# Optimization experiments

Measured on AMD Instinct MI355X. Metric: run time of the kernel, lower is better.

Reference implementation:

```python
import jax, jax.numpy as jnp
import numpy as np

EPS = 1e-5

def _ln(x, g, b):
    m = jnp.mean(x, axis=-1, keepdims=True)
    v = jnp.mean((x - m) ** 2, axis=-1, keepdims=True)
    return (x - m) * jax.lax.rsqrt(v + EPS) * g + b


def setup_inputs() -> dict:
    key = jax.random.key(0)
    B, T, C, H, A = 4, 1024, 1024, 16, 64
    ks = jax.random.split(key, 16)
    s = 0.02
    inp = {
        "x": jax.random.normal(ks[0], (B, T, C), jnp.float32),
        "ln1_g": jnp.ones((C,), jnp.float32), "ln1_b": jnp.zeros((C,), jnp.float32),
        "ln2_g": jnp.ones((C,), jnp.float32), "ln2_b": jnp.zeros((C,), jnp.float32),
        "ln3_g": jnp.ones((C,), jnp.float32), "ln3_b": jnp.zeros((C,), jnp.float32),
        "wq": jax.random.normal(ks[1], (C, C), jnp.float32) * s, "bq": jnp.zeros((C,), jnp.float32),
        "wk": jax.random.normal(ks[2], (C, C), jnp.float32) * s, "bk": jnp.zeros((C,), jnp.float32),
        "wv": jax.random.normal(ks[3], (C, C), jnp.float32) * s, "bv": jnp.zeros((C,), jnp.float32),
        "wo": jax.random.normal(ks[4], (C, C), jnp.float32) * s, "bo": jnp.zeros((C,), jnp.float32),
        "w1": jax.random.normal(ks[5], (C, 4 * C), jnp.float32) * s, "b1": jnp.zeros((4 * C,), jnp.float32),
        "w2": jax.random.normal(ks[6], (4 * C, C), jnp.float32) * s, "b2": jnp.zeros((C,), jnp.float32),
        "wd": jax.random.normal(ks[7], (C, A), jnp.float32) * 1e-4, "bd": jnp.zeros((A,), jnp.float32),
        "wu": jax.random.normal(ks[8], (A, C), jnp.float32) * 1e-4, "bu": jnp.zeros((C,), jnp.float32),
    }
    return inp


def _block(x, ln1_g, ln1_b, ln2_g, ln2_b, ln3_g, ln3_b,
           wq, bq, wk, bk, wv, bv, wo, bo, w1, b1, w2, b2, wd, bd, wu, bu):
    B, T, C = x.shape
    H = 16
    D = C // H
    normed = _ln(x, ln3_g, ln3_b)  # ln3 of original input, used by adapter

    # --- causal self-attention on ln1(x) ---
    h = _ln(x, ln1_g, ln1_b)
    q = (h @ wq + bq).reshape(B, T, H, D)
    k = (h @ wk + bk).reshape(B, T, H, D)
    v = (h @ wv + bv).reshape(B, T, H, D)
    att = jnp.einsum('bqhd,bkhd->bhqk', q, k) * (1.0 / np.sqrt(D))
    causal = jnp.tril(jnp.ones((T, T), bool))
    att = jnp.where(causal, att, -jnp.inf)
    att = jax.nn.softmax(att, axis=-1)
    y = jnp.einsum('bhqk,bkhd->bqhd', att, v).reshape(B, T, C)
    attn_out = y @ wo + bo

    hidden = x + attn_out
    # --- MLP on ln2(hidden) ---
    m = _ln(hidden, ln2_g, ln2_b)
    mlp_out = jax.nn.gelu(m @ w1 + b1, approximate=False) @ w2 + b2
    forward_states = hidden + mlp_out

    # --- adapter on ln3(original x) ---
    a = jax.nn.relu(normed @ wd + bd) @ wu + bu

    # dropout is identity (p=0 / eval)
    return hidden + forward_states + a


def reference(x, ln1_g, ln1_b, ln2_g, ln2_b, ln3_g, ln3_b,
              wq, bq, wk, bk, wv, bv, wo, bo, w1, b1, w2, b2, wd, bd, wu, bu):
    return _block(x, ln1_g, ln1_b, ln2_g, ln2_b, ln3_g, ln3_b,
                  wq, bq, wk, bk, wv, bv, wo, bo, w1, b1, w2, b2, wd, bd, wu, bu)
```

## Files before the change

kernel.cpp:

```cpp
#include <hip/hip_runtime.h>

typedef unsigned short u16;
typedef __bf16 bf16x8 __attribute__((ext_vector_type(8)));
typedef u16    u16x8  __attribute__((ext_vector_type(8)));
typedef float  f32x4  __attribute__((ext_vector_type(4)));

__device__ __forceinline__ u16 f2bf(float f) {
    union { float f; unsigned u; } x{f};
    unsigned r = x.u + 0x7fffu + ((x.u >> 16) & 1u);
    return (u16)(r >> 16);
}
__device__ __forceinline__ float bf2f(u16 h) {
    union { unsigned u; float f; } x{(unsigned)h << 16};
    return x.f;
}

__device__ __forceinline__ f32x4 mfma16(bf16x8 a, bf16x8 b, f32x4 c) {
    return __builtin_amdgcn_mfma_f32_16x16x32_bf16(a, b, c, 0, 0, 0);
}

__device__ __forceinline__ void async_ld16(const void* g, void* l) {
    __builtin_amdgcn_global_load_lds(
        (const __attribute__((address_space(1))) unsigned int*)g,
        (__attribute__((address_space(3))) unsigned int*)l, 16, 0, 0);
}

struct PrepParams {
    const float* src[8];
    u16* dst[8];
    int K[8], N[8];
    int pfx[9];
    const float *bq, *bk, *bv;
    float* bqkv;
};

__global__ void prep_kernel(PrepParams p) {
    const int b = blockIdx.x;
    if (b >= p.pfx[8]) {
        int i = (b - p.pfx[8]) * 256 + threadIdx.x;
        p.bqkv[i] = i < 1024 ? p.bq[i] : (i < 2048 ? p.bk[i - 1024] : p.bv[i - 2048]);
        return;
    }
    int j = 0;
    while (b >= p.pfx[j + 1]) ++j;
    const float* __restrict__ in = p.src[j];
    u16* __restrict__ out = p.dst[j];
    const int K = p.K[j], N = p.N[j];
    const int local = b - p.pfx[j];
    const int tx = N >> 6;
    const int n0 = (local % tx) * 64, k0 = (local / tx) * 64;

    __shared__ float tile[64][65];
    const int tid = threadIdx.x;
    const int rr = tid >> 4, cc = tid & 15;
#pragma unroll
    for (int it = 0; it < 4; ++it) {
        const int r = rr + it * 16;
        float4 v = *(const float4*)(in + (long)(k0 + r) * N + n0 + cc * 4);
        tile[r][cc * 4 + 0] = v.x; tile[r][cc * 4 + 1] = v.y;
        tile[r][cc * 4 + 2] = v.z; tile[r][cc * 4 + 3] = v.w;
    }
    __syncthreads();
#pragma unroll
    for (int it = 0; it < 4; ++it) {
        const int n = rr + it * 16;
        ushort4 o;
        o.x = f2bf(tile[cc * 4 + 0][n]);
        o.y = f2bf(tile[cc * 4 + 1][n]);
        o.z = f2bf(tile[cc * 4 + 2][n]);
        o.w = f2bf(tile[cc * 4 + 3][n]);
        *(ushort4*)(out + (long)(n0 + n) * K + k0 + cc * 4) = o;
    }
}

__global__ void ln_dual_kernel(const float* __restrict__ x,
                               const float* __restrict__ g1, const float* __restrict__ b1,
                               const float* __restrict__ g3, const float* __restrict__ b3,
                               u16* __restrict__ out1, u16* __restrict__ out3) {
    const int row = blockIdx.x;
    const long base = (long)row * 1024;
    const int t = threadIdx.x;
    float4 v = ((const float4*)(x + base))[t];
    float s = v.x + v.y + v.z + v.w;
    float ss = v.x * v.x + v.y * v.y + v.z * v.z + v.w * v.w;
    for (int o = 32; o > 0; o >>= 1) { s += __shfl_down(s, o); ss += __shfl_down(ss, o); }
    __shared__ float red[8];
    if ((t & 63) == 0) { red[t >> 6] = s; red[(t >> 6) + 4] = ss; }
    __syncthreads();
    float sum = red[0] + red[1] + red[2] + red[3];
    float sq  = red[4] + red[5] + red[6] + red[7];
    const float mean = sum * (1.f / 1024.f);
    const float rstd = rsqrtf(sq * (1.f / 1024.f) - mean * mean + 1e-5f);
    float4 G1 = ((const float4*)g1)[t], B1 = ((const float4*)b1)[t];
    float4 G3 = ((const float4*)g3)[t], B3 = ((const float4*)b3)[t];
    float n0 = (v.x - mean) * rstd, n1 = (v.y - mean) * rstd;
    float n2 = (v.z - mean) * rstd, n3 = (v.w - mean) * rstd;
    ushort4 o1, o3;
    o1.x = f2bf(n0 * G1.x + B1.x); o1.y = f2bf(n1 * G1.y + B1.y);
    o1.z = f2bf(n2 * G1.z + B1.z); o1.w = f2bf(n3 * G1.w + B1.w);
    o3.x = f2bf(n0 * G3.x + B3.x); o3.y = f2bf(n1 * G3.y + B3.y);
    o3.z = f2bf(n2 * G3.z + B3.z); o3.w = f2bf(n3 * G3.w + B3.w);
    ((ushort4*)(out1 + base))[t] = o1;
    ((ushort4*)(out3 + base))[t] = o3;
}

__global__ void ln_single_kernel(const float* __restrict__ x,
                                 const float* __restrict__ g, const float* __restrict__ b,
                                 u16* __restrict__ out) {
    const int row = blockIdx.x;
    const long base = (long)row * 1024;
    const int t = threadIdx.x;
    float4 v = ((const float4*)(x + base))[t];
    float s = v.x + v.y + v.z + v.w;
    float ss = v.x * v.x + v.y * v.y + v.z * v.z + v.w * v.w;
    for (int o = 32; o > 0; o >>= 1) { s += __shfl_down(s, o); ss += __shfl_down(ss, o); }
    __shared__ float red[8];
    if ((t & 63) == 0) { red[t >> 6] = s; red[(t >> 6) + 4] = ss; }
    __syncthreads();
    float sum = red[0] + red[1] + red[2] + red[3];
    float sq  = red[4] + red[5] + red[6] + red[7];
    const float mean = sum * (1.f / 1024.f);
    const float rstd = rsqrtf(sq * (1.f / 1024.f) - mean * mean + 1e-5f);
    float4 G = ((const float4*)g)[t], B = ((const float4*)b)[t];
    ushort4 o;
    o.x = f2bf((v.x - mean) * rstd * G.x + B.x);
    o.y = f2bf((v.y - mean) * rstd * G.y + B.y);
    o.z = f2bf((v.z - mean) * rstd * G.z + B.z);
    o.w = f2bf((v.w - mean) * rstd * G.w + B.w);
    ((ushort4*)(out + base))[t] = o;
}

__global__ void transpose_v(const u16* __restrict__ qkv, u16* __restrict__ vT) {
    const int bh = blockIdx.z, b = bh >> 4, hh = bh & 15;
    const int t0 = blockIdx.x * 32, d0 = blockIdx.y * 32;
    __shared__ u16 tile[32][33];
    const u16* src = qkv + (long)(b * 1024) * 3072 + 2048 + hh * 64;
    for (int i = threadIdx.y; i < 32; i += 8)
        tile[i][threadIdx.x] = src[(long)(t0 + i) * 3072 + d0 + threadIdx.x];
    __syncthreads();
    u16* dst = vT + (long)bh * 64 * 1024;
    for (int i = threadIdx.y; i < 32; i += 8)
        dst[(long)(d0 + i) * 1024 + t0 + threadIdx.x] = tile[threadIdx.x][i];
}

__global__ void reduce_out4(float* __restrict__ out, const u16* __restrict__ p,
                            const float* __restrict__ b2) {
    const long base = (long)blockIdx.x * 1024;
    const int t = threadIdx.x;
    float4 sum = {0.f, 0.f, 0.f, 0.f};
#pragma unroll
    for (int z = 0; z < 4; ++z) {
        ushort4 q = ((const ushort4*)(p + (long)z * (4096L * 1024) + base))[t];
        sum.x += bf2f(q.x); sum.y += bf2f(q.y);
        sum.z += bf2f(q.z); sum.w += bf2f(q.w);
    }
    float4 bias = ((const float4*)b2)[t];
    float4 o = ((const float4*)(out + base))[t];
    o.x += sum.x + bias.x; o.y += sum.y + bias.y;
    o.z += sum.z + bias.z; o.w += sum.w + bias.w;
    ((float4*)(out + base))[t] = o;
}

template <typename Epi>
__global__ __launch_bounds__(128, 2)
void gemm_big(const u16* __restrict__ A, const u16* __restrict__ Bt,
              int N, int K, int ld, Epi epi) {
    constexpr int AE = 128 * 32;
    __shared__ u16 sm[2][AE + AE];
    const int tid = threadIdx.x;
    const int wid = tid >> 6, lane = tid & 63;
    const int lr = lane & 15, lh = lane >> 4;
    const int m0 = blockIdx.y * 128, n0 = blockIdx.x * 128;
    const long k0g = (long)blockIdx.z * K;
    const int wn = wid * 64;

    const int cr = lane >> 2, lq = lane & 3;
    long aoff[4], boff[4];
    int lA[4], lB[4];
#pragma unroll
    for (int c = 0; c < 4; ++c) {
        const int r = wid * 64 + c * 16 + cr;
        const int q = lq ^ (r & 3) ^ ((r >> 2) & 3);
        aoff[c] = (long)(m0 + r) * ld + k0g + q * 8;
        boff[c] = (long)(n0 + r) * ld + k0g + q * 8;
        lA[c] = (wid * 4 + c) * 512;
        lB[c] = AE + (wid * 4 + c) * 512;
    }
    const int qoff = ((lh ^ (lr & 3) ^ ((lr >> 2) & 3)) & 3) * 8;

    f32x4 acc[8][4] = {};
    const int nk = K / 32;

    auto stage = [&](int kt) {
        const long ko = (long)kt * 32;
        u16* s = sm[kt & 1];
#pragma unroll
        for (int c = 0; c < 4; ++c) {
            async_ld16(A + aoff[c] + ko, s + lA[c]);
            async_ld16(Bt + boff[c] + ko, s + lB[c]);
        }
    };
    auto compute = [&](int kt) {
        const u16* sA = sm[kt & 1];
        const u16* sB = sA + AE;
        bf16x8 bfr[4];
#pragma unroll
        for (int j = 0; j < 4; ++j)
            bfr[j] = *(const bf16x8*)(sB + (wn + j * 16 + lr) * 32 + qoff);
#pragma unroll
        for (int i = 0; i < 8; ++i) {
            bf16x8 af = *(const bf16x8*)(sA + (i * 16 + lr) * 32 + qoff);
#pragma unroll
            for (int j = 0; j < 4; ++j)
                acc[i][j] = mfma16(af, bfr[j], acc[i][j]);
        }
    };

    stage(0);
    __syncthreads();
    for (int kt = 0; kt < nk; ++kt) {
        if (kt + 1 < nk) stage(kt + 1);
        compute(kt);
        __syncthreads();
    }

#pragma unroll
    for (int i = 0; i < 8; ++i)
#pragma unroll
        for (int j = 0; j < 4; ++j) {
            const int col = n0 + wn + j * 16 + lr;
#pragma unroll
            for (int r = 0; r < 4; ++r)
                epi(m0 + i * 16 + lh * 4 + r, col, acc[i][j][r]);
        }
}

template <typename Epi>
__global__ __launch_bounds__(256, 4)
void gemm_64(const u16* __restrict__ A, const u16* __restrict__ Bt,
             int N, int K, int ld, Epi epi) {
    constexpr int AE = 128 * 32;
    constexpr int BE = 64 * 32;
    __shared__ u16 sm[2][AE + BE];
    const int tid = threadIdx.x;
    const int m0 = blockIdx.y * 128;
    const int n0 = blockIdx.x * 64;
    const long k0g = (long)blockIdx.z * K;
    const int wid = tid >> 6, lane = tid & 63;
    const int lr = lane & 15, lh = lane >> 4;
    const int wm = wid * 32;

    const int cr = lane >> 2, lq = lane & 3;
    const int ra0 = wid * 32 + cr, ra1 = ra0 + 16;
    const int qa0 = lq ^ (ra0 & 3) ^ ((ra0 >> 2) & 3);
    const int qa1 = lq ^ (ra1 & 3) ^ ((ra1 >> 2) & 3);
    const long aoff0 = (long)(m0 + ra0) * ld + k0g + qa0 * 8;
    const long aoff1 = (long)(m0 + ra1) * ld + k0g + qa1 * 8;
    const int la0 = wid * 1024, la1 = la0 + 512;

    const int rb = wid * 16 + cr;
    const int qb = lq ^ (rb & 3) ^ ((rb >> 2) & 3);
    const long boff0 = (long)min(n0 + rb, N - 1) * ld + k0g + qb * 8;
    const int lb0 = AE + wid * 512;

    const int qoff = ((lh ^ (lr & 3) ^ ((lr >> 2) & 3)) & 3) * 8;

    f32x4 acc[2][4] = {};
    const int nk = K / 32;

    auto stage = [&](int kt) {
        const long ko = (long)kt * 32;
        u16* s = sm[kt & 1];
        async_ld16(A + aoff0 + ko, s + la0);
        async_ld16(A + aoff1 + ko, s + la1);
        async_ld16(Bt + boff0 + ko, s + lb0);
    };
    auto compute = [&](int kt) {
        const u16* sA = sm[kt & 1];
        const u16* sB = sA + AE;
        bf16x8 af[2], bfr[4];
#pragma unroll
        for (int i = 0; i < 2; ++i)
            af[i] = *(const bf16x8*)(sA + (wm + i * 16 + lr) * 32 + qoff);
#pragma unroll
        for (int j = 0; j < 4; ++j)
            bfr[j] = *(const bf16x8*)(sB + (j * 16 + lr) * 32 + qoff);
#pragma unroll
        for (int i = 0; i < 2; ++i)
#pragma unroll
            for (int j = 0; j < 4; ++j)
                acc[i][j] = mfma16(af[i], bfr[j], acc[i][j]);
    };

    stage(0);
    __syncthreads();
    for (int kt = 0; kt < nk; ++kt) {
        if (kt + 1 < nk) stage(kt + 1);
        compute(kt);
        __syncthreads();
    }

#pragma unroll
    for (int i = 0; i < 2; ++i)
#pragma unroll
        for (int j = 0; j < 4; ++j) {
            const int col = n0 + j * 16 + lr;
            if (col < N) {
#pragma unroll
                for (int r = 0; r < 4; ++r) {
                    const int row = m0 + wm + i * 16 + lh * 4 + r;
                    epi(row, col, acc[i][j][r]);
                }
            }
        }
}

struct EpiBF16Bias {
    u16* out; const float* bias; int ldo;
    __device__ void operator()(int r, int c, float v) const {
        out[(long)r * ldo + c] = f2bf(v + bias[c]);
    }
};
struct EpiResid {
    float* hidden; const float* bias; const float* x;
    __device__ void operator()(int r, int c, float v) const {
        long i = (long)r * 1024 + c; hidden[i] = v + bias[c] + x[i];
    }
};
struct EpiGelu {
    u16* out; const float* bias;
    __device__ void operator()(int r, int c, float v) const {
        float x = v + bias[c];
        float u2 = x * (1.5957691216f + 0.0713548162726f * x * x);
        float g = x / (1.f + __expf(-u2));
        out[(long)r * 4096 + c] = f2bf(g);
    }
};
struct EpiReluBF16 {
    u16* out; const float* bias;
    __device__ void operator()(int r, int c, float v) const {
        out[(long)r * 64 + c] = f2bf(fmaxf(v + bias[c], 0.f));
    }
};
struct EpiAdapter {
    float* out; const float* bias; const float* hidden;
    __device__ void operator()(int r, int c, float v) const {
        long i = (long)r * 1024 + c; out[i] = 2.f * hidden[i] + v + bias[c];
    }
};
struct EpiStoreSplit {
    u16* p;
    __device__ void operator()(int r, int c, float v) const {
        p[(long)blockIdx.z * (4096L * 1024) + (long)r * 1024 + c] = f2bf(v);
    }
};

__global__ __launch_bounds__(256, 2)
void attn_kernel(const u16* __restrict__ qkv, const u16* __restrict__ vT,
                 u16* __restrict__ y) {
    const int bh = blockIdx.x, b = bh >> 4, hh = bh & 15;
    const int q0 = blockIdx.y * 128;
    const int tid = threadIdx.x, wid = tid >> 6, lane = tid & 63;
    const int lr = lane & 15, lh = lane >> 4;
    const int qw = q0 + wid * 32;

    __shared__ u16 smK[64 * 72];
    __shared__ u16 smV[64 * 72];
    __shared__ u16 smP[4 * 32 * 72];
    u16* pw = smP + wid * (32 * 72);

    const u16* qbase = qkv + (long)(b * 1024) * 3072 + hh * 64;
    const u16* kbase = qbase + 1024;
    const u16* vbase = vT + (long)bh * 64 * 1024;

    bf16x8 a_q[2][2];
#pragma unroll
    for (int mt = 0; mt < 2; ++mt)
#pragma unroll
        for (int ks = 0; ks < 2; ++ks) {
            uint4 t = *(const uint4*)(qbase + (long)(qw + mt * 16 + lr) * 3072 + ks * 32 + lh * 8);
            a_q[mt][ks] = __builtin_bit_cast(bf16x8, t);
        }

    bf16x8 ones;
    { u16x8 t = {0x3F80, 0x3F80, 0x3F80, 0x3F80, 0x3F80, 0x3F80, 0x3F80, 0x3F80};
      ones = __builtin_bit_cast(bf16x8, t); }

    f32x4 o_acc[2][4] = {};
    f32x4 l_acc[2] = {};
    f32x4 m_run[2] = {{-1e30f, -1e30f, -1e30f, -1e30f}, {-1e30f, -1e30f, -1e30f, -1e30f}};

    const int ntiles = q0 / 64 + 2;
    const int ck = tid >> 3, cs = (tid & 7) * 8;
    const int ck2 = (tid + 256) >> 3, cs2 = ((tid + 256) & 7) * 8;
    for (int kt = 0; kt < ntiles; ++kt) {
        const int k0 = kt * 64;
        __syncthreads();
        {
            uint4 kv0 = *(const uint4*)(kbase + (long)(k0 + ck) * 3072 + cs);
            uint4 kv1 = *(const uint4*)(kbase + (long)(k0 + ck2) * 3072 + cs2);
            *(uint4*)(smK + ck * 72 + cs) = kv0;
            *(uint4*)(smK + ck2 * 72 + cs2) = kv1;
            uint4 vv0 = *(const uint4*)(vbase + (long)ck * 1024 + k0 + cs);
            uint4 vv1 = *(const uint4*)(vbase + (long)ck2 * 1024 + k0 + cs2);
            *(uint4*)(smV + ck * 72 + cs) = vv0;
            *(uint4*)(smV + ck2 * 72 + cs2) = vv1;
        }
        __syncthreads();
        if (k0 > qw + 31) continue;

        bf16x8 bK[4][2];
#pragma unroll
        for (int nt = 0; nt < 4; ++nt)
#pragma unroll
            for (int ks = 0; ks < 2; ++ks)
                bK[nt][ks] = *(const bf16x8*)(smK + (nt * 16 + lr) * 72 + ks * 32 + lh * 8);

        f32x4 s[2][4];
#pragma unroll
        for (int mt = 0; mt < 2; ++mt)
#pragma unroll
            for (int nt = 0; nt < 4; ++nt) {
                f32x4 z = {0.f, 0.f, 0.f, 0.f};
                z = mfma16(a_q[mt][0], bK[nt][0], z);
                z = mfma16(a_q[mt][1], bK[nt][1], z);
                s[mt][nt] = z;
            }
#pragma unroll
        for (int mt = 0; mt < 2; ++mt) {
            const int qb = qw + mt * 16 + lh * 4;
#pragma unroll
            for (int nt = 0; nt < 4; ++nt) {
                const int kkg = k0 + nt * 16 + lr;
#pragma unroll
                for (int r = 0; r < 4; ++r) {
                    float v = s[mt][nt][r] * 0.125f;
                    if (kkg > qb + r) v = -1e30f;
                    s[mt][nt][r] = v;
                }
            }
        }
#pragma unroll
        for (int mt = 0; mt < 2; ++mt) {
            f32x4 mx = s[mt][0];
#pragma unroll
            for (int nt = 1; nt < 4; ++nt)
#pragma unroll
                for (int r = 0; r < 4; ++r) mx[r] = fmaxf(mx[r], s[mt][nt][r]);
#pragma unroll
            for (int xm = 1; xm < 16; xm <<= 1)
#pragma unroll
                for (int r = 0; r < 4; ++r) mx[r] = fmaxf(mx[r], __shfl_xor(mx[r], xm));
            f32x4 mnew, alpha;
#pragma unroll
            for (int r = 0; r < 4; ++r) {
                mnew[r] = fmaxf(m_run[mt][r], mx[r]);
                alpha[r] = __expf(m_run[mt][r] - mnew[r]);
            }
            m_run[mt] = mnew;
            l_acc[mt] *= alpha;
#pragma unroll
            for (int dt = 0; dt < 4; ++dt) o_acc[mt][dt] *= alpha;
#pragma unroll
            for (int nt = 0; nt < 4; ++nt)
#pragma unroll
                for (int r = 0; r < 4; ++r)
                    s[mt][nt][r] = __expf(s[mt][nt][r] - mnew[r]);
#pragma unroll
            for (int nt = 0; nt < 4; ++nt)
#pragma unroll
                for (int r = 0; r < 4; ++r)
                    pw[(mt * 16 + lh * 4 + r) * 72 + nt * 16 + lr] = f2bf(s[mt][nt][r]);
        }
        bf16x8 vf[4][2];
#pragma unroll
        for (int dt = 0; dt < 4; ++dt)
#pragma unroll
            for (int ks = 0; ks < 2; ++ks)
                vf[dt][ks] = *(const bf16x8*)(smV + (dt * 16 + lr) * 72 + ks * 32 + lh * 8);
#pragma unroll
        for (int mt = 0; mt < 2; ++mt) {
            bf16x8 pf0 = *(const bf16x8*)(pw + (mt * 16 + lr) * 72 + lh * 8);
            bf16x8 pf1 = *(const bf16x8*)(pw + (mt * 16 + lr) * 72 + 32 + lh * 8);
            l_acc[mt] = mfma16(pf0, ones, l_acc[mt]);
            l_acc[mt] = mfma16(pf1, ones, l_acc[mt]);
#pragma unroll
            for (int dt = 0; dt < 4; ++dt) {
                o_acc[mt][dt] = mfma16(pf0, vf[dt][0], o_acc[mt][dt]);
                o_acc[mt][dt] = mfma16(pf1, vf[dt][1], o_acc[mt][dt]);
            }
        }
    }
#pragma unroll
    for (int mt = 0; mt < 2; ++mt) {
        f32x4 linv;
#pragma unroll
        for (int r = 0; r < 4; ++r) linv[r] = 1.f / l_acc[mt][r];
#pragma unroll
        for (int dt = 0; dt < 4; ++dt) {
#pragma unroll
            for (int r = 0; r < 4; ++r) {
                const int tok = b * 1024 + qw + mt * 16 + lh * 4 + r;
                y[(long)tok * 1024 + hh * 64 + dt * 16 + lr] = f2bf(o_acc[mt][dt][r] * linv[r]);
            }
        }
    }
}

extern "C" void kernel_launch(void* const* d_in, const int* in_sizes, int n_in,
                              void* d_out, int out_size, void* d_ws, size_t ws_size,
                              hipStream_t stream) {
    const float* x    = (const float*)d_in[0];
    const float* ln1g = (const float*)d_in[1];
    const float* ln1b = (const float*)d_in[2];
    const float* ln2g = (const float*)d_in[3];
    const float* ln2b = (const float*)d_in[4];
    const float* ln3g = (const float*)d_in[5];
    const float* ln3b = (const float*)d_in[6];
    const float* wq = (const float*)d_in[7];  const float* bq = (const float*)d_in[8];
    const float* wk = (const float*)d_in[9];  const float* bk = (const float*)d_in[10];
    const float* wv = (const float*)d_in[11]; const float* bv = (const float*)d_in[12];
    const float* wo = (const float*)d_in[13]; const float* bo = (const float*)d_in[14];
    const float* w1 = (const float*)d_in[15]; const float* b1 = (const float*)d_in[16];
    const float* w2 = (const float*)d_in[17]; const float* b2 = (const float*)d_in[18];
    const float* wd = (const float*)d_in[19]; const float* bd = (const float*)d_in[20];
    const float* wu = (const float*)d_in[21]; const float* bu = (const float*)d_in[22];
    float* out = (float*)d_out;

    char* base = (char*)d_ws;
    size_t off = 0;
    auto carve = [&](size_t bytes) -> char* {
        char* p = base + off; off += (bytes + 255) & ~(size_t)255; return p;
    };
    u16* qkv_wt = (u16*)carve(3072L * 1024 * 2);
    u16* wo_t   = (u16*)carve(1024L * 1024 * 2);
    u16* w1_t   = (u16*)carve(4096L * 1024 * 2);
    u16* w2_t   = (u16*)carve(1024L * 4096 * 2);
    u16* wd_t   = (u16*)carve(64L * 1024 * 2);
    u16* wu_t   = (u16*)carve(1024L * 64 * 2);
    float* bqkv = (float*)carve(3072L * 4);
    u16* hbuf   = (u16*)carve(4096L * 1024 * 2);
    u16* nrm    = (u16*)carve(4096L * 1024 * 2);
    u16* qkvb   = (u16*)carve(4096L * 3072 * 2);
    u16* vT     = (u16*)carve(64L * 64 * 1024 * 2);
    u16* ybuf   = (u16*)carve(4096L * 1024 * 2);
    float* hid  = (float*)carve(4096L * 1024 * 4);
    u16* mbuf   = (u16*)carve(4096L * 1024 * 2);
    u16* act    = (u16*)carve(4096L * 4096 * 2);
    u16* t1     = (u16*)carve(4096L * 64 * 2);
    u16* part   = (u16*)carve(4L * 4096 * 1024 * 2);

    PrepParams pp;
    pp.src[0] = wq; pp.dst[0] = qkv_wt;                 pp.K[0] = 1024; pp.N[0] = 1024;
    pp.src[1] = wk; pp.dst[1] = qkv_wt + 1024L * 1024;  pp.K[1] = 1024; pp.N[1] = 1024;
    pp.src[2] = wv; pp.dst[2] = qkv_wt + 2048L * 1024;  pp.K[2] = 1024; pp.N[2] = 1024;
    pp.src[3] = wo; pp.dst[3] = wo_t;                   pp.K[3] = 1024; pp.N[3] = 1024;
    pp.src[4] = w1; pp.dst[4] = w1_t;                   pp.K[4] = 1024; pp.N[4] = 4096;
    pp.src[5] = w2; pp.dst[5] = w2_t;                   pp.K[5] = 4096; pp.N[5] = 1024;
    pp.src[6] = wd; pp.dst[6] = wd_t;                   pp.K[6] = 1024; pp.N[6] = 64;
    pp.src[7] = wu; pp.dst[7] = wu_t;                   pp.K[7] = 64;   pp.N[7] = 1024;
    int acc_blocks = 0;
    for (int j = 0; j < 8; ++j) {
        pp.pfx[j] = acc_blocks;
        acc_blocks += (pp.N[j] >> 6) * (pp.K[j] >> 6);
    }
    pp.pfx[8] = acc_blocks;
    pp.bq = bq; pp.bk = bk; pp.bv = bv; pp.bqkv = bqkv;
    prep_kernel<<<acc_blocks + 12, 256, 0, stream>>>(pp);

    ln_dual_kernel<<<4096, 256, 0, stream>>>(x, ln1g, ln1b, ln3g, ln3b, hbuf, nrm);

    gemm_big<<<dim3(24, 32), 128, 0, stream>>>(hbuf, qkv_wt, 3072, 1024, 1024,
                                               EpiBF16Bias{qkvb, bqkv, 3072});
    transpose_v<<<dim3(32, 2, 64), dim3(32, 8), 0, stream>>>(qkvb, vT);
    attn_kernel<<<dim3(64, 8), 256, 0, stream>>>(qkvb, vT, ybuf);
    gemm_64<<<dim3(16, 32), 256, 0, stream>>>(ybuf, wo_t, 1024, 1024, 1024,
                                              EpiResid{hid, bo, x});
    ln_single_kernel<<<4096, 256, 0, stream>>>(hid, ln2g, ln2b, mbuf);
    gemm_big<<<dim3(32, 32), 128, 0, stream>>>(mbuf, w1_t, 4096, 1024, 1024,
                                               EpiGelu{act, b1});
    gemm_64<<<dim3(1, 32), 256, 0, stream>>>(nrm, wd_t, 64, 1024, 1024,
                                             EpiReluBF16{t1, bd});
    gemm_64<<<dim3(16, 32), 256, 0, stream>>>(t1, wu_t, 1024, 64, 64,
                                              EpiAdapter{out, bu, hid});
    gemm_big<<<dim3(8, 32, 4), 128, 0, stream>>>(act, w2_t, 1024, 1024, 4096,
                                                 EpiStoreSplit{part});
    reduce_out4<<<4096, 256, 0, stream>>>(out, part, b2);
}
```

Before: 403.7 us.

## Use 256x256 GEMM tiles, fuse LN into prep, split-K wo with fused LN2

Replaces the 128x128 GEMM with a 256x256-tile, 4-wave kernel holding 8x8 accumulators per wave, to raise data reuse per LDS load. The ln1/ln3 LayerNorm is folded into the weight-prep launch as extra blocks, which removes one launch. The wo projection now uses split-K into bf16 partials, and a new kernel reduces them, adds the residual and bias, and applies ln2 in one pass. The risks are heavy register pressure from 64 accumulator tiles and low occupancy, since the QKV GEMM launches only 192 blocks. The bf16 partials also add rounding to the attention output.

```diff
diff --git a/kernel.cpp b/kernel.cpp
--- a/kernel.cpp
+++ b/kernel.cpp
@@ -32,12 +32,44 @@
     int pfx[9];
     const float *bq, *bk, *bv;
     float* bqkv;
+    const float *x, *g1, *b1, *g3, *b3;
+    u16 *o1, *o3;
 };
 
 __global__ void prep_kernel(PrepParams p) {
     const int b = blockIdx.x;
+    const int t = threadIdx.x;
+    __shared__ float tile[64][65];
+    __shared__ float red[8];
+
+    if (b >= p.pfx[8] + 12) {
+        const int row = b - p.pfx[8] - 12;
+        const long base = (long)row * 1024;
+        float4 v = ((const float4*)(p.x + base))[t];
+        float s = v.x + v.y + v.z + v.w;
+        float ss = v.x * v.x + v.y * v.y + v.z * v.z + v.w * v.w;
+        for (int o = 32; o > 0; o >>= 1) { s += __shfl_down(s, o); ss += __shfl_down(ss, o); }
+        if ((t & 63) == 0) { red[t >> 6] = s; red[(t >> 6) + 4] = ss; }
+        __syncthreads();
+        float sum = red[0] + red[1] + red[2] + red[3];
+        float sq  = red[4] + red[5] + red[6] + red[7];
+        const float mean = sum * (1.f / 1024.f);
+        const float rstd = rsqrtf(sq * (1.f / 1024.f) - mean * mean + 1e-5f);
+        float4 G1 = ((const float4*)p.g1)[t], B1 = ((const float4*)p.b1)[t];
+        float4 G3 = ((const float4*)p.g3)[t], B3 = ((const float4*)p.b3)[t];
+        float n0 = (v.x - mean) * rstd, n1 = (v.y - mean) * rstd;
+        float n2 = (v.z - mean) * rstd, n3 = (v.w - mean) * rstd;
+        ushort4 o1, o3;
+        o1.x = f2bf(n0 * G1.x + B1.x); o1.y = f2bf(n1 * G1.y + B1.y);
+        o1.z = f2bf(n2 * G1.z + B1.z); o1.w = f2bf(n3 * G1.w + B1.w);
+        o3.x = f2bf(n0 * G3.x + B3.x); o3.y = f2bf(n1 * G3.y + B3.y);
+        o3.z = f2bf(n2 * G3.z + B3.z); o3.w = f2bf(n3 * G3.w + B3.w);
+        ((ushort4*)(p.o1 + base))[t] = o1;
+        ((ushort4*)(p.o3 + base))[t] = o3;
+        return;
+    }
     if (b >= p.pfx[8]) {
-        int i = (b - p.pfx[8]) * 256 + threadIdx.x;
+        int i = (b - p.pfx[8]) * 256 + t;
         p.bqkv[i] = i < 1024 ? p.bq[i] : (i < 2048 ? p.bk[i - 1024] : p.bv[i - 2048]);
         return;
     }
@@ -49,10 +81,7 @@
     const int local = b - p.pfx[j];
     const int tx = N >> 6;
     const int n0 = (local % tx) * 64, k0 = (local / tx) * 64;
-
-    __shared__ float tile[64][65];
-    const int tid = threadIdx.x;
-    const int rr = tid >> 4, cc = tid & 15;
+    const int rr = t >> 4, cc = t & 15;
 #pragma unroll
     for (int it = 0; it < 4; ++it) {
         const int r = rr + it * 16;
@@ -71,63 +100,6 @@
         o.w = f2bf(tile[cc * 4 + 3][n]);
         *(ushort4*)(out + (long)(n0 + n) * K + k0 + cc * 4) = o;
     }
-}
-
-__global__ void ln_dual_kernel(const float* __restrict__ x,
-                               const float* __restrict__ g1, const float* __restrict__ b1,
-                               const float* __restrict__ g3, const float* __restrict__ b3,
-                               u16* __restrict__ out1, u16* __restrict__ out3) {
-    const int row = blockIdx.x;
-    const long base = (long)row * 1024;
-    const int t = threadIdx.x;
-    float4 v = ((const float4*)(x + base))[t];
-    float s = v.x + v.y + v.z + v.w;
-    float ss = v.x * v.x + v.y * v.y + v.z * v.z + v.w * v.w;
-    for (int o = 32; o > 0; o >>= 1) { s += __shfl_down(s, o); ss += __shfl_down(ss, o); }
-    __shared__ float red[8];
-    if ((t & 63) == 0) { red[t >> 6] = s; red[(t >> 6) + 4] = ss; }
-    __syncthreads();
-    float sum = red[0] + red[1] + red[2] + red[3];
-    float sq  = red[4] + red[5] + red[6] + red[7];
-    const float mean = sum * (1.f / 1024.f);
-    const float rstd = rsqrtf(sq * (1.f / 1024.f) - mean * mean + 1e-5f);
-    float4 G1 = ((const float4*)g1)[t], B1 = ((const float4*)b1)[t];
-    float4 G3 = ((const float4*)g3)[t], B3 = ((const float4*)b3)[t];
-    float n0 = (v.x - mean) * rstd, n1 = (v.y - mean) * rstd;
-    float n2 = (v.z - mean) * rstd, n3 = (v.w - mean) * rstd;
-    ushort4 o1, o3;
-    o1.x = f2bf(n0 * G1.x + B1.x); o1.y = f2bf(n1 * G1.y + B1.y);
-    o1.z = f2bf(n2 * G1.z + B1.z); o1.w = f2bf(n3 * G1.w + B1.w);
-    o3.x = f2bf(n0 * G3.x + B3.x); o3.y = f2bf(n1 * G3.y + B3.y);
-    o3.z = f2bf(n2 * G3.z + B3.z); o3.w = f2bf(n3 * G3.w + B3.w);
-    ((ushort4*)(out1 + base))[t] = o1;
-    ((ushort4*)(out3 + base))[t] = o3;
-}
-
-__global__ void ln_single_kernel(const float* __restrict__ x,
-                                 const float* __restrict__ g, const float* __restrict__ b,
-                                 u16* __restrict__ out) {
-    const int row = blockIdx.x;
-    const long base = (long)row * 1024;
-    const int t = threadIdx.x;
-    float4 v = ((const float4*)(x + base))[t];
-    float s = v.x + v.y + v.z + v.w;
-    float ss = v.x * v.x + v.y * v.y + v.z * v.z + v.w * v.w;
-    for (int o = 32; o > 0; o >>= 1) { s += __shfl_down(s, o); ss += __shfl_down(ss, o); }
-    __shared__ float red[8];
-    if ((t & 63) == 0) { red[t >> 6] = s; red[(t >> 6) + 4] = ss; }
-    __syncthreads();
-    float sum = red[0] + red[1] + red[2] + red[3];
-    float sq  = red[4] + red[5] + red[6] + red[7];
-    const float mean = sum * (1.f / 1024.f);
-    const float rstd = rsqrtf(sq * (1.f / 1024.f) - mean * mean + 1e-5f);
-    float4 G = ((const float4*)g)[t], B = ((const float4*)b)[t];
-    ushort4 o;
-    o.x = f2bf((v.x - mean) * rstd * G.x + B.x);
-    o.y = f2bf((v.y - mean) * rstd * G.y + B.y);
-    o.z = f2bf((v.z - mean) * rstd * G.z + B.z);
-    o.w = f2bf((v.w - mean) * rstd * G.w + B.w);
-    ((ushort4*)(out + base))[t] = o;
 }
 
 __global__ void transpose_v(const u16* __restrict__ qkv, u16* __restrict__ vT) {
@@ -143,6 +115,41 @@
         dst[(long)(d0 + i) * 1024 + t0 + threadIdx.x] = tile[threadIdx.x][i];
 }
 
+__global__ void reduce_wo_ln(const u16* __restrict__ part, const float* __restrict__ x,
+                             const float* __restrict__ bo, const float* __restrict__ g,
+                             const float* __restrict__ bb, float* __restrict__ hid,
+                             u16* __restrict__ mbuf) {
+    const int row = blockIdx.x;
+    const long base = (long)row * 1024;
+    const int t = threadIdx.x;
+    float4 h = ((const float4*)(x + base))[t];
+    float4 bo4 = ((const float4*)bo)[t];
+    h.x += bo4.x; h.y += bo4.y; h.z += bo4.z; h.w += bo4.w;
+#pragma unroll
+    for (int z = 0; z < 4; ++z) {
+        ushort4 q = ((const ushort4*)(part + (long)z * (4096L * 1024) + base))[t];
+        h.x += bf2f(q.x); h.y += bf2f(q.y); h.z += bf2f(q.z); h.w += bf2f(q.w);
+    }
+    ((float4*)(hid + base))[t] = h;
+    float s = h.x + h.y + h.z + h.w;
+    float ss = h.x * h.x + h.y * h.y + h.z * h.z + h.w * h.w;
+    for (int o = 32; o > 0; o >>= 1) { s += __shfl_down(s, o); ss += __shfl_down(ss, o); }
+    __shared__ float red[8];
+    if ((t & 63) == 0) { red[t >> 6] = s; red[(t >> 6) + 4] = ss; }
+    __syncthreads();
+    float sum = red[0] + red[1] + red[2] + red[3];
+    float sq  = red[4] + red[5] + red[6] + red[7];
+    const float mean = sum * (1.f / 1024.f);
+    const float rstd = rsqrtf(sq * (1.f / 1024.f) - mean * mean + 1e-5f);
+    float4 G = ((const float4*)g)[t], B = ((const float4*)bb)[t];
+    ushort4 o;
+    o.x = f2bf((h.x - mean) * rstd * G.x + B.x);
+    o.y = f2bf((h.y - mean) * rstd * G.y + B.y);
+    o.z = f2bf((h.z - mean) * rstd * G.z + B.z);
+    o.w = f2bf((h.w - mean) * rstd * G.w + B.w);
+    ((ushort4*)(mbuf + base))[t] = o;
+}
+
 __global__ void reduce_out4(float* __restrict__ out, const u16* __restrict__ p,
                             const float* __restrict__ b2) {
     const long base = (long)blockIdx.x * 1024;
@@ -162,24 +169,24 @@
 }
 
 template <typename Epi>
-__global__ __launch_bounds__(128, 2)
-void gemm_big(const u16* __restrict__ A, const u16* __restrict__ Bt,
-              int N, int K, int ld, Epi epi) {
-    constexpr int AE = 128 * 32;
+__global__ __launch_bounds__(256, 1)
+void gemm_256(const u16* __restrict__ A, const u16* __restrict__ Bt,
+              int K, int ld, Epi epi) {
+    constexpr int AE = 256 * 32;
     __shared__ u16 sm[2][AE + AE];
     const int tid = threadIdx.x;
     const int wid = tid >> 6, lane = tid & 63;
     const int lr = lane & 15, lh = lane >> 4;
-    const int m0 = blockIdx.y * 128, n0 = blockIdx.x * 128;
+    const int m0 = blockIdx.y * 256, n0 = blockIdx.x * 256;
     const long k0g = (long)blockIdx.z * K;
-    const int wn = wid * 64;
+    const int wm = (wid >> 1) * 128, wn = (wid & 1) * 128;
 
     const int cr = lane >> 2, lq = lane & 3;
     long aoff[4], boff[4];
     int lA[4], lB[4];
 #pragma unroll
     for (int c = 0; c < 4; ++c) {
-        const int r = wid * 64 + c * 16 + cr;
+        const int r = (wid * 4 + c) * 16 + cr;
         const int q = lq ^ (r & 3) ^ ((r >> 2) & 3);
         aoff[c] = (long)(m0 + r) * ld + k0g + q * 8;
         boff[c] = (long)(n0 + r) * ld + k0g + q * 8;
@@ -188,7 +195,7 @@
     }
     const int qoff = ((lh ^ (lr & 3) ^ ((lr >> 2) & 3)) & 3) * 8;
 
-    f32x4 acc[8][4] = {};
+    f32x4 acc[8][8] = {};
     const int nk = K / 32;
 
     auto stage = [&](int kt) {
@@ -203,15 +210,15 @@
     auto compute = [&](int kt) {
         const u16* sA = sm[kt & 1];
         const u16* sB = sA + AE;
-        bf16x8 bfr[4];
-#pragma unroll
-        for (int j = 0; j < 4; ++j)
+        bf16x8 bfr[8];
+#pragma unroll
+        for (int j = 0; j < 8; ++j)
             bfr[j] = *(const bf16x8*)(sB + (wn + j * 16 + lr) * 32 + qoff);
 #pragma unroll
         for (int i = 0; i < 8; ++i) {
-            bf16x8 af = *(const bf16x8*)(sA + (i * 16 + lr) * 32 + qoff);
-#pragma unroll
-            for (int j = 0; j < 4; ++j)
+            bf16x8 af = *(const bf16x8*)(sA + (wm + i * 16 + lr) * 32 + qoff);
+#pragma unroll
+            for (int j = 0; j < 8; ++j)
                 acc[i][j] = mfma16(af, bfr[j], acc[i][j]);
         }
     };
@@ -227,11 +234,11 @@
 #pragma unroll
     for (int i = 0; i < 8; ++i)
 #pragma unroll
-        for (int j = 0; j < 4; ++j) {
+        for (int j = 0; j < 8; ++j) {
             const int col = n0 + wn + j * 16 + lr;
 #pragma unroll
             for (int r = 0; r < 4; ++r)
-                epi(m0 + i * 16 + lh * 4 + r, col, acc[i][j][r]);
+                epi(m0 + wm + i * 16 + lh * 4 + r, col, acc[i][j][r]);
         }
 }
 
@@ -319,12 +326,6 @@
     u16* out; const float* bias; int ldo;
     __device__ void operator()(int r, int c, float v) const {
         out[(long)r * ldo + c] = f2bf(v + bias[c]);
-    }
-};
-struct EpiResid {
-    float* hidden; const float* bias; const float* x;
-    __device__ void operator()(int r, int c, float v) const {
-        long i = (long)r * 1024 + c; hidden[i] = v + bias[c] + x[i];
     }
 };
 struct EpiGelu {
@@ -566,24 +567,24 @@
     }
     pp.pfx[8] = acc_blocks;
     pp.bq = bq; pp.bk = bk; pp.bv = bv; pp.bqkv = bqkv;
-    prep_kernel<<<acc_blocks + 12, 256, 0, stream>>>(pp);
-
-    ln_dual_kernel<<<4096, 256, 0, stream>>>(x, ln1g, ln1b, ln3g, ln3b, hbuf, nrm);
-
-    gemm_big<<<dim3(24, 32), 128, 0, stream>>>(hbuf, qkv_wt, 3072, 1024, 1024,
+    pp.x = x; pp.g1 = ln1g; pp.b1 = ln1b; pp.g3 = ln3g; pp.b3 = ln3b;
+    pp.o1 = hbuf; pp.o3 = nrm;
+    prep_kernel<<<acc_blocks + 12 + 4096, 256, 0, stream>>>(pp);
+
+    gemm_256<<<dim3(12, 16), 256, 0, stream>>>(hbuf, qkv_wt, 1024, 1024,
                                                EpiBF16Bias{qkvb, bqkv, 3072});
     transpose_v<<<dim3(32, 2, 64), dim3(32, 8), 0, stream>>>(qkvb, vT);
     attn_kernel<<<dim3(64, 8), 256, 0, stream>>>(qkvb, vT, ybuf);
-    gemm_64<<<dim3(16, 32), 256, 0, stream>>>(ybuf, wo_t, 1024, 1024, 1024,
-                                              EpiResid{hid, bo, x});
-    ln_single_kernel<<<4096, 256, 0, stream>>>(hid, ln2g, ln2b, mbuf);
-    gemm_big<<<dim3(32, 32), 128, 0, stream>>>(mbuf, w1_t, 4096, 1024, 1024,
+    gemm_256<<<dim3(4, 16, 4), 256, 0, stream>>>(ybuf, wo_t, 256, 1024,
+                                                 EpiStoreSplit{part});
+    reduce_wo_ln<<<4096, 256, 0, stream>>>(part, x, bo, ln2g, ln2b, hid, mbuf);
+    gemm_256<<<dim3(16, 16), 256, 0, stream>>>(mbuf, w1_t, 1024, 1024,
                                                EpiGelu{act, b1});
     gemm_64<<<dim3(1, 32), 256, 0, stream>>>(nrm, wd_t, 64, 1024, 1024,
                                              EpiReluBF16{t1, bd});
     gemm_64<<<dim3(16, 32), 256, 0, stream>>>(t1, wu_t, 1024, 64, 64,
                                               EpiAdapter{out, bu, hid});
-    gemm_big<<<dim3(8, 32, 4), 128, 0, stream>>>(act, w2_t, 1024, 1024, 4096,
+    gemm_256<<<dim3(4, 16, 4), 256, 0, stream>>>(act, w2_t, 1024, 4096,
                                                  EpiStoreSplit{part});
     reduce_out4<<<4096, 256, 0, stream>>>(out, part, b2);
 }
```

After: 421.6 us. +4.5%, slower.
